# Performance work log

Hardware: AMD Instinct MI355X
Metric: run time of the kernel (lower is better)

## Reference

```python
import jax, jax.numpy as jnp
import numpy as np

NUM_NODES = 100000
NUM_EDGES = 1600000
NUM_GRAPHS = 128
D_IN, D_H1, D_H2, N_CLS = 128, 16, 128, 2


def gcn_conv(x, src, dst, W, b, num_nodes):
    # PyG GCNConv: linear transform, add self-loops, sym-normalized scatter-add
    h = x @ W  # [N, out]
    loop = jnp.arange(num_nodes, dtype=src.dtype)
    s = jnp.concatenate([src, loop])
    d = jnp.concatenate([dst, loop])
    deg = jax.ops.segment_sum(jnp.ones_like(d, dtype=h.dtype), d, num_segments=num_nodes)
    dinv = jax.lax.rsqrt(jnp.maximum(deg, 1.0))  # self-loops guarantee deg>=1
    norm = dinv[s] * dinv[d]  # [E+N]
    msg = h[s] * norm[:, None]  # gather + scale
    out = jax.ops.segment_sum(msg, d, num_segments=num_nodes)  # scatter-add
    return out + b


def setup_inputs() -> dict:
    key = jax.random.key(0)
    ks = jax.random.split(key, 12)
    x = jax.random.normal(ks[0], (NUM_NODES, D_IN), dtype=jnp.float32)
    edge_index = jax.random.randint(ks[1], (2, NUM_EDGES), 0, NUM_NODES, dtype=jnp.int64)
    batch = jax.random.randint(ks[2], (NUM_NODES,), 0, NUM_GRAPHS, dtype=jnp.int64)
    def glorot(k, shp):
        lim = np.sqrt(6.0 / (shp[0] + shp[1]))
        return jax.random.uniform(k, shp, dtype=jnp.float32, minval=-lim, maxval=lim)
    return {
        "x": x, "edge_index": edge_index, "batch": batch,
        "W1": glorot(ks[3], (D_IN, D_H1)), "b1": jnp.zeros((D_H1,), jnp.float32),
        "W2": glorot(ks[4], (D_H1, D_H2)), "b2": jnp.zeros((D_H2,), jnp.float32),
        "LW1": glorot(ks[5], (D_H2, D_H2)), "Lb1": jnp.zeros((D_H2,), jnp.float32),
        "LW2": glorot(ks[6], (D_H2, N_CLS)), "Lb2": jnp.zeros((N_CLS,), jnp.float32),
    }


def reference(x, edge_index, batch, W1, b1, W2, b2, LW1, Lb1, LW2, Lb2):
    src, dst = edge_index[0], edge_index[1]
    h = jax.nn.relu(gcn_conv(x, src, dst, W1, b1, NUM_NODES))
    h = jax.nn.relu(gcn_conv(h, src, dst, W2, b2, NUM_NODES))
    # global mean pool over graphs
    sums = jax.ops.segment_sum(h, batch, num_segments=NUM_GRAPHS)  # [G, D_H2]
    cnts = jax.ops.segment_sum(jnp.ones((h.shape[0],), h.dtype), batch, num_segments=NUM_GRAPHS)
    pooled = sums / jnp.maximum(cnts, 1.0)[:, None]
    z = jax.nn.relu(pooled @ LW1 + Lb1)
    z = z @ LW2 + Lb2
    return jax.nn.log_softmax(z, axis=-1)  # [G, num_classes]
```

## Files before the change

kernel.cpp:

```cpp
#include <hip/hip_runtime.h>

typedef unsigned int u32;

#define N_NODES  100000
#define N_EDGES  1600000
#define N_GRAPHS 128

#define NPB      200
#define NBUK     500
#define CHUNK    8192
#define NCHUNK   196
#define NHIST    (NBUK*NCHUNK)
#define NBLKA    383
#define CAP      6144

__global__ __launch_bounds__(512) void k_hist1(const int* __restrict__ dst, const int* __restrict__ batch,
                                               int* __restrict__ hist, int* __restrict__ bhist) {
    int t = threadIdx.x, b = blockIdx.x;
    if (b < NCHUNK) {
        __shared__ int lh[NBUK];
        for (int i = t; i < NBUK; i += 512) lh[i] = 0;
        __syncthreads();
        int base = b * CHUNK;
        #pragma unroll
        for (int it = 0; it < CHUNK / 512; ++it) {
            int e = base + it * 512 + t;
            if (e < N_EDGES) atomicAdd(&lh[dst[e] / NPB], 1);
        }
        __syncthreads();
        for (int i = t; i < NBUK; i += 512) hist[i * NCHUNK + b] = lh[i];
    } else {
        __shared__ int bh[N_GRAPHS];
        if (t < N_GRAPHS) bh[t] = 0;
        __syncthreads();
        int n = (b - NCHUNK) * 512 + t;
        if (n < N_NODES) atomicAdd(&bh[batch[n]], 1);
        __syncthreads();
        if (t < N_GRAPHS) atomicAdd(&bhist[t], bh[t]);
    }
}

__global__ __launch_bounds__(256) void k_scanA1(const int* __restrict__ hist, int* __restrict__ asum) {
    __shared__ int sh[256];
    int t = threadIdx.x, i = blockIdx.x * 256 + t;
    sh[t] = (i < NHIST) ? hist[i] : 0;
    __syncthreads();
    for (int off = 128; off > 0; off >>= 1) {
        if (t < off) sh[t] += sh[t + off];
        __syncthreads();
    }
    if (t == 0) asum[blockIdx.x] = sh[0];
}

__global__ __launch_bounds__(512) void k_scanA2(const int* __restrict__ asum, int* __restrict__ asumOff,
                                                const int* __restrict__ bhist, int* __restrict__ boff,
                                                int* __restrict__ bcur) {
    __shared__ int s1[512], s2[512];
    int t = threadIdx.x;
    int v = (t < NBLKA) ? asum[t] : 0;
    s1[t] = v; __syncthreads();
    int* pa = s1; int* pb = s2;
    for (int off = 1; off < 512; off <<= 1) {
        int x = pa[t];
        if (t >= off) x += pa[t - off];
        pb[t] = x; __syncthreads();
        int* tmp = pa; pa = pb; pb = tmp;
    }
    if (t < NBLKA) asumOff[t] = pa[t] - v;
    __syncthreads();
    int hv = (t < N_GRAPHS) ? bhist[t] : 0;
    pa[t] = hv; __syncthreads();
    int* qa = pa; int* qb = pb;
    for (int off = 1; off < 512; off <<= 1) {
        int x = qa[t];
        if (t >= off) x += qa[t - off];
        qb[t] = x; __syncthreads();
        int* tmp = qa; qa = qb; qb = tmp;
    }
    if (t < N_GRAPHS) { int e = qa[t] - hv; boff[t] = e; bcur[t] = e; }
    if (t == 0) boff[N_GRAPHS] = N_NODES;
}

__global__ __launch_bounds__(256) void k_scanA3(int* __restrict__ hist, const int* __restrict__ asumOff) {
    __shared__ int a1[256], a2[256];
    int t = threadIdx.x, i = blockIdx.x * 256 + t;
    int v = (i < NHIST) ? hist[i] : 0;
    a1[t] = v; __syncthreads();
    int* pa = a1; int* pb = a2;
    for (int off = 1; off < 256; off <<= 1) {
        int x = pa[t];
        if (t >= off) x += pa[t - off];
        pb[t] = x; __syncthreads();
        int* tmp = pa; pa = pb; pb = tmp;
    }
    if (i < NHIST) hist[i] = pa[t] - v + asumOff[blockIdx.x];
}

__global__ __launch_bounds__(512) void k_bin(const int* __restrict__ src, const int* __restrict__ dst,
                                             const int* __restrict__ hist, u32* __restrict__ packed,
                                             const int* __restrict__ batch, int* __restrict__ bcur,
                                             int* __restrict__ nodeS) {
    int t = threadIdx.x, b = blockIdx.x;
    if (b < NCHUNK) {
        __shared__ int cur5[NBUK];
        for (int i = t; i < NBUK; i += 512) cur5[i] = hist[i * NCHUNK + b];
        __syncthreads();
        int base = b * CHUNK;
        #pragma unroll
        for (int it = 0; it < CHUNK / 512; ++it) {
            int e = base + it * 512 + t;
            if (e < N_EDGES) {
                int d = dst[e], s = src[e];
                int bk = d / NPB;
                int pos = atomicAdd(&cur5[bk], 1);
                packed[pos] = ((u32)(d - bk * NPB) << 24) | (u32)s;
            }
        }
    } else {
        int n = (b - NCHUNK) * 512 + t;
        if (n < N_NODES) {
            int pos = atomicAdd(&bcur[batch[n]], 1);
            nodeS[pos] = n;
        }
    }
}

__global__ __launch_bounds__(256) void k_locCSR(const u32* __restrict__ packed, const int* __restrict__ hist,
                                                int* __restrict__ row, float* __restrict__ dinv,
                                                int* __restrict__ srcS) {
    __shared__ u32 lp[CAP];
    __shared__ int sbuf[CAP];
    __shared__ int cnt[NPB];
    __shared__ int s1[256], s2[256];
    int b = blockIdx.x, t = threadIdx.x;
    int start = hist[b * NCHUNK];
    int end   = (b == NBUK - 1) ? N_EDGES : hist[(b + 1) * NCHUNK];
    int len = end - start;
    for (int i = t; i < NPB; i += 256) cnt[i] = 0;
    __syncthreads();
    bool cached = (len <= CAP);
    if (cached) {
        for (int i = t; i < len; i += 256) {
            u32 p = packed[start + i];
            lp[i] = p;
            atomicAdd(&cnt[p >> 24], 1);
        }
    } else {
        for (int i = t; i < len; i += 256) {
            u32 p = packed[start + i];
            atomicAdd(&cnt[p >> 24], 1);
        }
    }
    __syncthreads();
    int v = (t < NPB) ? cnt[t] : 0;
    s1[t] = v; __syncthreads();
    int* pa = s1; int* pb = s2;
    for (int off = 1; off < 256; off <<= 1) {
        int x = pa[t];
        if (t >= off) x += pa[t - off];
        pb[t] = x; __syncthreads();
        int* tmp = pa; pa = pb; pb = tmp;
    }
    int excl = pa[t] - v;
    if (t < NPB) {
        row[b * NPB + t]  = start + excl;
        dinv[b * NPB + t] = rsqrtf((float)(v + 1));
    }
    if (b == NBUK - 1 && t == 0) row[N_NODES] = N_EDGES;
    __syncthreads();
    if (t < NPB) cnt[t] = excl;
    __syncthreads();
    if (cached) {
        for (int i = t; i < len; i += 256) {
            u32 p = lp[i];
            int lpos = atomicAdd(&cnt[p >> 24], 1);
            sbuf[lpos] = (int)(p & 0xFFFFFFu);
        }
        __syncthreads();
        for (int i = t; i < len; i += 256) srcS[start + i] = sbuf[i];
    } else {
        for (int i = t; i < len; i += 256) {
            u32 p = packed[start + i];
            int lpos = atomicAdd(&cnt[p >> 24], 1);
            srcS[start + lpos] = (int)(p & 0xFFFFFFu);
        }
    }
}

__global__ __launch_bounds__(256) void k_gemm1(const float* __restrict__ x, const float* __restrict__ W1,
                                               const float* __restrict__ dinv, float* __restrict__ t1s) {
    __shared__ float w[128 * 16];
    __shared__ float xs[16][132];
    int t = threadIdx.x;
    {
        const float4* wv = (const float4*)W1;
        ((float4*)w)[t * 2]     = wv[t * 2];
        ((float4*)w)[t * 2 + 1] = wv[t * 2 + 1];
    }
    int base = blockIdx.x * 16;
    {
        const float4* xv = (const float4*)(x + (size_t)base * 128);
        #pragma unroll
        for (int q = 0; q < 2; ++q) {
            int i4 = t * 2 + q;
            float4 v = xv[i4];
            int idx = i4 * 4;
            *((float4*)&xs[idx >> 7][idx & 127]) = v;
        }
    }
    __syncthreads();
    int nl = t >> 4, j = t & 15;
    int n = base + nl;
    const float4* xr = (const float4*)&xs[nl][0];
    float acc = 0.f;
    #pragma unroll
    for (int k4 = 0; k4 < 32; ++k4) {
        float4 v = xr[k4];
        acc += v.x * w[(k4 * 4 + 0) * 16 + j];
        acc += v.y * w[(k4 * 4 + 1) * 16 + j];
        acc += v.z * w[(k4 * 4 + 2) * 16 + j];
        acc += v.w * w[(k4 * 4 + 3) * 16 + j];
    }
    t1s[n * 16 + j] = dinv[n] * acc;
}

template <int LAYER>
__global__ __launch_bounds__(256) void k_gather(const int* __restrict__ row, const int* __restrict__ srcS,
                                                const float4* __restrict__ hs4, const float* __restrict__ dinv,
                                                const float* __restrict__ b1, float4* __restrict__ out4) {
    int t = threadIdx.x;
    int q = t & 3;
    int n = blockIdx.x * 64 + (t >> 2);
    if (n >= N_NODES) return;
    int r0 = row[n], r1 = row[n + 1];
    float4 a0 = hs4[(size_t)n * 4 + q];
    float4 a1 = {0.f, 0.f, 0.f, 0.f};
    float4 a2 = {0.f, 0.f, 0.f, 0.f};
    float4 a3 = {0.f, 0.f, 0.f, 0.f};
    int i = r0;
    for (; i + 4 <= r1; i += 4) {
        int s0 = srcS[i], s1 = srcS[i + 1], s2 = srcS[i + 2], s3 = srcS[i + 3];
        float4 v0 = hs4[(size_t)s0 * 4 + q];
        float4 v1 = hs4[(size_t)s1 * 4 + q];
        float4 v2 = hs4[(size_t)s2 * 4 + q];
        float4 v3 = hs4[(size_t)s3 * 4 + q];
        a0.x += v0.x; a0.y += v0.y; a0.z += v0.z; a0.w += v0.w;
        a1.x += v1.x; a1.y += v1.y; a1.z += v1.z; a1.w += v1.w;
        a2.x += v2.x; a2.y += v2.y; a2.z += v2.z; a2.w += v2.w;
        a3.x += v3.x; a3.y += v3.y; a3.z += v3.z; a3.w += v3.w;
    }
    for (; i < r1; ++i) {
        int s = srcS[i];
        float4 v = hs4[(size_t)s * 4 + q];
        a0.x += v.x; a0.y += v.y; a0.z += v.z; a0.w += v.w;
    }
    float sx = (a0.x + a1.x) + (a2.x + a3.x);
    float sy = (a0.y + a1.y) + (a2.y + a3.y);
    float sz = (a0.z + a1.z) + (a2.z + a3.z);
    float sw = (a0.w + a1.w) + (a2.w + a3.w);
    float dv = dinv[n];
    float4 r;
    if (LAYER == 1) {
        const float4 bb = ((const float4*)b1)[q];
        r.x = dv * fmaxf(dv * sx + bb.x, 0.f);
        r.y = dv * fmaxf(dv * sy + bb.y, 0.f);
        r.z = dv * fmaxf(dv * sz + bb.z, 0.f);
        r.w = dv * fmaxf(dv * sw + bb.w, 0.f);
    } else {
        r.x = dv * sx; r.y = dv * sy; r.z = dv * sz; r.w = dv * sw;
    }
    out4[(size_t)n * 4 + q] = r;
}

__global__ __launch_bounds__(256) void k_pool(const float* __restrict__ q2, const float* __restrict__ W2,
                                              const float* __restrict__ b2, const int* __restrict__ nodeS,
                                              const int* __restrict__ batch, float* __restrict__ sums) {
    __shared__ float w[16 * 128];
    __shared__ float bsh[128];
    __shared__ float rows[64][16];
    __shared__ int   gid[64];
    int t = threadIdx.x;
    {
        const float4* wv = (const float4*)W2;
        ((float4*)w)[t * 2]     = wv[t * 2];
        ((float4*)w)[t * 2 + 1] = wv[t * 2 + 1];
    }
    if (t < 128) bsh[t] = b2[t];
    int base = blockIdx.x * 64;
    {
        int which = t >> 2, qq = t & 3;
        int idx = base + which;
        if (idx < N_NODES) {
            int node = nodeS[idx];
            if (qq == 0) gid[which] = batch[node];
            float4 v = ((const float4*)q2)[(size_t)node * 4 + qq];
            *(float4*)&rows[which][qq * 4] = v;
        }
    }
    __syncthreads();
    int half = t >> 7, j = t & 127;
    float acc = 0.f;
    int curg = -1;
    for (int it = 0; it < 32; ++it) {
        int wh = half * 32 + it;
        int idx = base + wh;
        if (idx >= N_NODES) break;
        int g = gid[wh];
        if (g != curg) {
            if (curg >= 0) atomicAdd(&sums[curg * 128 + j], acc);
            curg = g; acc = 0.f;
        }
        float a = bsh[j];
        #pragma unroll
        for (int kk = 0; kk < 16; ++kk) a += rows[wh][kk] * w[kk * 128 + j];
        acc += fmaxf(a, 0.f);
    }
    if (curg >= 0) atomicAdd(&sums[curg * 128 + j], acc);
}

__global__ __launch_bounds__(128) void k_head(const float* __restrict__ sums, const int* __restrict__ boff,
                                              const float* __restrict__ LW1, const float* __restrict__ Lb1,
                                              const float* __restrict__ LW2, const float* __restrict__ Lb2,
                                              float* __restrict__ out) {
    __shared__ float srow[128];
    __shared__ float z1s[128];
    __shared__ float zz[2];
    int g = blockIdx.x, t = threadIdx.x;
    int cnt = boff[g + 1] - boff[g];
    float rc = 1.0f / fmaxf((float)cnt, 1.0f);
    srow[t] = sums[g * 128 + t] * rc;
    __syncthreads();
    float a = Lb1[t];
    for (int k = 0; k < 128; ++k) a += srow[k] * LW1[k * 128 + t];
    z1s[t] = fmaxf(a, 0.f);
    __syncthreads();
    if (t < 2) {
        float z = Lb2[t];
        for (int jj = 0; jj < 128; ++jj) z += z1s[jj] * LW2[jj * 2 + t];
        zz[t] = z;
    }
    __syncthreads();
    if (t < 2) {
        float m = fmaxf(zz[0], zz[1]);
        float lse = m + logf(expf(zz[0] - m) + expf(zz[1] - m));
        out[g * 2 + t] = zz[t] - lse;
    }
}

extern "C" void kernel_launch(void* const* d_in, const int* in_sizes, int n_in,
                              void* d_out, int out_size, void* d_ws, size_t ws_size,
                              hipStream_t stream) {
    const float* x   = (const float*)d_in[0];
    const int* ei    = (const int*)d_in[1];
    const int* batch = (const int*)d_in[2];
    const float* W1  = (const float*)d_in[3];
    const float* b1  = (const float*)d_in[4];
    const float* W2  = (const float*)d_in[5];
    const float* b2  = (const float*)d_in[6];
    const float* LW1 = (const float*)d_in[7];
    const float* Lb1 = (const float*)d_in[8];
    const float* LW2 = (const float*)d_in[9];
    const float* Lb2 = (const float*)d_in[10];
    const int* src = ei;
    const int* dst = ei + N_EDGES;

    char* ws = (char*)d_ws;
    int*   bhist   = (int*)(ws);
    float* sums    = (float*)(ws + 512);
    int*   bcur    = (int*)(ws + 66048);
    int*   boff    = (int*)(ws + 66560);
    int*   asum    = (int*)(ws + 67584);
    int*   asumOff = (int*)(ws + 69120);
    int*   hist    = (int*)(ws + 70656);
    int*   row     = (int*)(ws + 462656);
    float* dinv    = (float*)(ws + 862784);
    int*   nodeS   = (int*)(ws + 1262784);
    int*   srcS    = (int*)(ws + 1662784);
    u32*   packed  = (u32*)(ws + 8062784);
    float* A       = (float*)(ws + 8062784);
    float* B       = (float*)(ws + 14462784);
    float* out     = (float*)d_out;

    hipMemsetAsync(ws, 0, 66048, stream);

    k_hist1    <<<NCHUNK + 196, 512, 0, stream>>>(dst, batch, hist, bhist);
    k_scanA1   <<<NBLKA,        256, 0, stream>>>(hist, asum);
    k_scanA2   <<<1,            512, 0, stream>>>(asum, asumOff, bhist, boff, bcur);
    k_scanA3   <<<NBLKA,        256, 0, stream>>>(hist, asumOff);
    k_bin      <<<NCHUNK + 196, 512, 0, stream>>>(src, dst, hist, packed, batch, bcur, nodeS);
    k_locCSR   <<<NBUK,         256, 0, stream>>>(packed, hist, row, dinv, srcS);
    k_gemm1    <<<6250,         256, 0, stream>>>(x, W1, dinv, A);
    k_gather<1><<<1563,         256, 0, stream>>>(row, srcS, (const float4*)A, dinv, b1, (float4*)B);
    k_gather<2><<<1563,         256, 0, stream>>>(row, srcS, (const float4*)B, dinv, b1, (float4*)A);
    k_pool     <<<1563,         256, 0, stream>>>(A, W2, b2, nodeS, batch, sums);
    k_head     <<<128,          128, 0, stream>>>(sums, boff, LW1, Lb1, LW2, Lb2, out);
}
```

Measured before the change: 320.6 us.

## Replace per-node CSR gather with bucketed shared-memory scatter and fp16 features

Drops the local CSR build (row offsets, sorted srcS). Propagation now runs directly over the dst-bucketed packed edge list, accumulating into shared memory per 200-node bucket with LDS float atomics, then flushing to a global fp32 accumulator with global atomics. Node features are stored in fp16 to halve gather bandwidth, and a separate epilogue kernel applies the layer-1 bias/relu and rezeroes the accumulator. In exchange it adds global atomics, a large extra memset, fp16 rounding error, and a non-deterministic summation order.

```diff
diff --git a/kernel.cpp b/kernel.cpp
--- a/kernel.cpp
+++ b/kernel.cpp
@@ -1,6 +1,8 @@
 #include <hip/hip_runtime.h>
+#include <hip/hip_fp16.h>
 
 typedef unsigned int u32;
+typedef unsigned short u16;
 
 #define N_NODES  100000
 #define N_EDGES  1600000
@@ -12,7 +14,10 @@
 #define NCHUNK   196
 #define NHIST    (NBUK*NCHUNK)
 #define NBLKA    383
-#define CAP      6144
+#define NBN      196
+
+__device__ __forceinline__ float h2f(u16 h) { return __half2float(__ushort_as_half(h)); }
+__device__ __forceinline__ u16 f2h(float f) { return __half_as_ushort(__float2half_rn(f)); }
 
 __global__ __launch_bounds__(512) void k_hist1(const int* __restrict__ dst, const int* __restrict__ batch,
                                                int* __restrict__ hist, int* __restrict__ bhist) {
@@ -82,11 +87,11 @@
 }
 
 __global__ __launch_bounds__(256) void k_scanA3(int* __restrict__ hist, const int* __restrict__ asumOff) {
-    __shared__ int a1[256], a2[256];
+    __shared__ int s1[256], s2[256];
     int t = threadIdx.x, i = blockIdx.x * 256 + t;
     int v = (i < NHIST) ? hist[i] : 0;
-    a1[t] = v; __syncthreads();
-    int* pa = a1; int* pb = a2;
+    s1[t] = v; __syncthreads();
+    int* pa = s1; int* pb = s2;
     for (int off = 1; off < 256; off <<= 1) {
         int x = pa[t];
         if (t >= off) x += pa[t - off];
@@ -125,70 +130,21 @@
     }
 }
 
-__global__ __launch_bounds__(256) void k_locCSR(const u32* __restrict__ packed, const int* __restrict__ hist,
-                                                int* __restrict__ row, float* __restrict__ dinv,
-                                                int* __restrict__ srcS) {
-    __shared__ u32 lp[CAP];
-    __shared__ int sbuf[CAP];
+__global__ __launch_bounds__(256) void k_degdinv(const u32* __restrict__ packed, const int* __restrict__ hist,
+                                                 float* __restrict__ dinv) {
     __shared__ int cnt[NPB];
-    __shared__ int s1[256], s2[256];
     int b = blockIdx.x, t = threadIdx.x;
+    for (int i = t; i < NPB; i += 256) cnt[i] = 0;
+    __syncthreads();
     int start = hist[b * NCHUNK];
-    int end   = (b == NBUK - 1) ? N_EDGES : hist[(b + 1) * NCHUNK];
-    int len = end - start;
-    for (int i = t; i < NPB; i += 256) cnt[i] = 0;
-    __syncthreads();
-    bool cached = (len <= CAP);
-    if (cached) {
-        for (int i = t; i < len; i += 256) {
-            u32 p = packed[start + i];
-            lp[i] = p;
-            atomicAdd(&cnt[p >> 24], 1);
-        }
-    } else {
-        for (int i = t; i < len; i += 256) {
-            u32 p = packed[start + i];
-            atomicAdd(&cnt[p >> 24], 1);
-        }
-    }
-    __syncthreads();
-    int v = (t < NPB) ? cnt[t] : 0;
-    s1[t] = v; __syncthreads();
-    int* pa = s1; int* pb = s2;
-    for (int off = 1; off < 256; off <<= 1) {
-        int x = pa[t];
-        if (t >= off) x += pa[t - off];
-        pb[t] = x; __syncthreads();
-        int* tmp = pa; pa = pb; pb = tmp;
-    }
-    int excl = pa[t] - v;
-    if (t < NPB) {
-        row[b * NPB + t]  = start + excl;
-        dinv[b * NPB + t] = rsqrtf((float)(v + 1));
-    }
-    if (b == NBUK - 1 && t == 0) row[N_NODES] = N_EDGES;
-    __syncthreads();
-    if (t < NPB) cnt[t] = excl;
-    __syncthreads();
-    if (cached) {
-        for (int i = t; i < len; i += 256) {
-            u32 p = lp[i];
-            int lpos = atomicAdd(&cnt[p >> 24], 1);
-            sbuf[lpos] = (int)(p & 0xFFFFFFu);
-        }
-        __syncthreads();
-        for (int i = t; i < len; i += 256) srcS[start + i] = sbuf[i];
-    } else {
-        for (int i = t; i < len; i += 256) {
-            u32 p = packed[start + i];
-            int lpos = atomicAdd(&cnt[p >> 24], 1);
-            srcS[start + lpos] = (int)(p & 0xFFFFFFu);
-        }
-    }
+    int end = (b == NBUK - 1) ? N_EDGES : hist[(b + 1) * NCHUNK];
+    for (int i = start + t; i < end; i += 256) atomicAdd(&cnt[packed[i] >> 24], 1);
+    __syncthreads();
+    if (t < NPB) dinv[b * NPB + t] = rsqrtf((float)(cnt[t] + 1));
 }
 
 __global__ __launch_bounds__(256) void k_gemm1(const float* __restrict__ x, const float* __restrict__ W1,
-                                               const float* __restrict__ dinv, float* __restrict__ t1s) {
+                                               const float* __restrict__ dinv, u16* __restrict__ hs1) {
     __shared__ float w[128 * 16];
     __shared__ float xs[16][132];
     int t = threadIdx.x;
@@ -221,60 +177,69 @@
         acc += v.z * w[(k4 * 4 + 2) * 16 + j];
         acc += v.w * w[(k4 * 4 + 3) * 16 + j];
     }
-    t1s[n * 16 + j] = dinv[n] * acc;
-}
-
-template <int LAYER>
-__global__ __launch_bounds__(256) void k_gather(const int* __restrict__ row, const int* __restrict__ srcS,
-                                                const float4* __restrict__ hs4, const float* __restrict__ dinv,
-                                                const float* __restrict__ b1, float4* __restrict__ out4) {
+    hs1[n * 16 + j] = f2h(dinv[n] * acc);
+}
+
+__global__ __launch_bounds__(512) void k_prop(const u32* __restrict__ packed, const int* __restrict__ hist,
+                                              const u16* __restrict__ hs, float* __restrict__ pacc) {
+    __shared__ float acc[NPB][17];
     int t = threadIdx.x;
-    int q = t & 3;
-    int n = blockIdx.x * 64 + (t >> 2);
+    int b = blockIdx.x >> 1, half = blockIdx.x & 1;
+    for (int i = t; i < NPB * 17; i += 512) (&acc[0][0])[i] = 0.f;
+    __syncthreads();
+    int start = hist[b * NCHUNK];
+    int end = (b == NBUK - 1) ? N_EDGES : hist[(b + 1) * NCHUNK];
+    int mid = start + ((end - start) >> 1);
+    int r0 = half ? mid : start;
+    int r1 = half ? end : mid;
+    int g = t >> 2, q = t & 3;
+    for (int i = r0 + g; i < r1; i += 128) {
+        u32 p = packed[i];
+        int dloc = (int)(p >> 24);
+        int s = (int)(p & 0xFFFFFFu);
+        ushort4 v = ((const ushort4*)hs)[s * 4 + q];
+        int c = q * 4;
+        atomicAdd(&acc[dloc][c + 0], h2f(v.x));
+        atomicAdd(&acc[dloc][c + 1], h2f(v.y));
+        atomicAdd(&acc[dloc][c + 2], h2f(v.z));
+        atomicAdd(&acc[dloc][c + 3], h2f(v.w));
+    }
+    __syncthreads();
+    int nb = b * NPB;
+    for (int i = t; i < NPB * 16; i += 512) {
+        int r = i >> 4, c = i & 15;
+        float v = acc[r][c];
+        if (v != 0.f) atomicAdd(&pacc[(nb + r) * 16 + c], v);
+    }
+}
+
+__global__ __launch_bounds__(256) void k_epi1(float* __restrict__ pacc, const u16* __restrict__ hs1,
+                                              const float* __restrict__ dinv, const float* __restrict__ b1,
+                                              u16* __restrict__ hs2) {
+    int gid = blockIdx.x * 256 + threadIdx.x;
+    int n = gid >> 2, q = gid & 3;
     if (n >= N_NODES) return;
-    int r0 = row[n], r1 = row[n + 1];
-    float4 a0 = hs4[(size_t)n * 4 + q];
-    float4 a1 = {0.f, 0.f, 0.f, 0.f};
-    float4 a2 = {0.f, 0.f, 0.f, 0.f};
-    float4 a3 = {0.f, 0.f, 0.f, 0.f};
-    int i = r0;
-    for (; i + 4 <= r1; i += 4) {
-        int s0 = srcS[i], s1 = srcS[i + 1], s2 = srcS[i + 2], s3 = srcS[i + 3];
-        float4 v0 = hs4[(size_t)s0 * 4 + q];
-        float4 v1 = hs4[(size_t)s1 * 4 + q];
-        float4 v2 = hs4[(size_t)s2 * 4 + q];
-        float4 v3 = hs4[(size_t)s3 * 4 + q];
-        a0.x += v0.x; a0.y += v0.y; a0.z += v0.z; a0.w += v0.w;
-        a1.x += v1.x; a1.y += v1.y; a1.z += v1.z; a1.w += v1.w;
-        a2.x += v2.x; a2.y += v2.y; a2.z += v2.z; a2.w += v2.w;
-        a3.x += v3.x; a3.y += v3.y; a3.z += v3.z; a3.w += v3.w;
-    }
-    for (; i < r1; ++i) {
-        int s = srcS[i];
-        float4 v = hs4[(size_t)s * 4 + q];
-        a0.x += v.x; a0.y += v.y; a0.z += v.z; a0.w += v.w;
-    }
-    float sx = (a0.x + a1.x) + (a2.x + a3.x);
-    float sy = (a0.y + a1.y) + (a2.y + a3.y);
-    float sz = (a0.z + a1.z) + (a2.z + a3.z);
-    float sw = (a0.w + a1.w) + (a2.w + a3.w);
+    int base = n * 4 + q;
+    float4 pv = ((float4*)pacc)[base];
+    ushort4 hv = ((const ushort4*)hs1)[base];
+    float4 bb = ((const float4*)b1)[q];
     float dv = dinv[n];
-    float4 r;
-    if (LAYER == 1) {
-        const float4 bb = ((const float4*)b1)[q];
-        r.x = dv * fmaxf(dv * sx + bb.x, 0.f);
-        r.y = dv * fmaxf(dv * sy + bb.y, 0.f);
-        r.z = dv * fmaxf(dv * sz + bb.z, 0.f);
-        r.w = dv * fmaxf(dv * sw + bb.w, 0.f);
-    } else {
-        r.x = dv * sx; r.y = dv * sy; r.z = dv * sz; r.w = dv * sw;
-    }
-    out4[(size_t)n * 4 + q] = r;
-}
-
-__global__ __launch_bounds__(256) void k_pool(const float* __restrict__ q2, const float* __restrict__ W2,
-                                              const float* __restrict__ b2, const int* __restrict__ nodeS,
-                                              const int* __restrict__ batch, float* __restrict__ sums) {
+    float h0 = fmaxf(dv * (pv.x + h2f(hv.x)) + bb.x, 0.f);
+    float h1 = fmaxf(dv * (pv.y + h2f(hv.y)) + bb.y, 0.f);
+    float h2 = fmaxf(dv * (pv.z + h2f(hv.z)) + bb.z, 0.f);
+    float h3 = fmaxf(dv * (pv.w + h2f(hv.w)) + bb.w, 0.f);
+    ushort4 o;
+    o.x = f2h(dv * h0); o.y = f2h(dv * h1); o.z = f2h(dv * h2); o.w = f2h(dv * h3);
+    ((ushort4*)hs2)[base] = o;
+    float4 z = {0.f, 0.f, 0.f, 0.f};
+    ((float4*)pacc)[base] = z;
+}
+
+__global__ __launch_bounds__(256) void k_pool(const float* __restrict__ pacc, const u16* __restrict__ hs2,
+                                              const float* __restrict__ dinv,
+                                              const float* __restrict__ W2, const float* __restrict__ b2,
+                                              const int* __restrict__ nodeS, const int* __restrict__ batch,
+                                              float* __restrict__ sums) {
     __shared__ float w[16 * 128];
     __shared__ float bsh[128];
     __shared__ float rows[64][16];
@@ -293,8 +258,13 @@
         if (idx < N_NODES) {
             int node = nodeS[idx];
             if (qq == 0) gid[which] = batch[node];
-            float4 v = ((const float4*)q2)[(size_t)node * 4 + qq];
-            *(float4*)&rows[which][qq * 4] = v;
+            float dv = dinv[node];
+            float4 pv = ((const float4*)pacc)[node * 4 + qq];
+            ushort4 hv = ((const ushort4*)hs2)[node * 4 + qq];
+            rows[which][qq * 4 + 0] = dv * (pv.x + h2f(hv.x));
+            rows[which][qq * 4 + 1] = dv * (pv.y + h2f(hv.y));
+            rows[which][qq * 4 + 2] = dv * (pv.z + h2f(hv.z));
+            rows[which][qq * 4 + 3] = dv * (pv.w + h2f(hv.w));
         }
     }
     __syncthreads();
@@ -367,31 +337,31 @@
     char* ws = (char*)d_ws;
     int*   bhist   = (int*)(ws);
     float* sums    = (float*)(ws + 512);
-    int*   bcur    = (int*)(ws + 66048);
-    int*   boff    = (int*)(ws + 66560);
-    int*   asum    = (int*)(ws + 67584);
-    int*   asumOff = (int*)(ws + 69120);
-    int*   hist    = (int*)(ws + 70656);
-    int*   row     = (int*)(ws + 462656);
-    float* dinv    = (float*)(ws + 862784);
-    int*   nodeS   = (int*)(ws + 1262784);
-    int*   srcS    = (int*)(ws + 1662784);
-    u32*   packed  = (u32*)(ws + 8062784);
-    float* A       = (float*)(ws + 8062784);
-    float* B       = (float*)(ws + 14462784);
+    float* pacc    = (float*)(ws + 66048);
+    int*   bcur    = (int*)(ws + 6466048);
+    int*   boff    = (int*)(ws + 6466560);
+    int*   asum    = (int*)(ws + 6467584);
+    int*   asumOff = (int*)(ws + 6469120);
+    int*   hist    = (int*)(ws + 6470656);
+    float* dinv    = (float*)(ws + 6862656);
+    int*   nodeS   = (int*)(ws + 7262656);
+    u32*   packed  = (u32*)(ws + 7662656);
+    u16*   hs1     = (u16*)(ws + 14062656);
+    u16*   hs2     = (u16*)(ws + 17262656);
     float* out     = (float*)d_out;
 
-    hipMemsetAsync(ws, 0, 66048, stream);
-
-    k_hist1    <<<NCHUNK + 196, 512, 0, stream>>>(dst, batch, hist, bhist);
-    k_scanA1   <<<NBLKA,        256, 0, stream>>>(hist, asum);
-    k_scanA2   <<<1,            512, 0, stream>>>(asum, asumOff, bhist, boff, bcur);
-    k_scanA3   <<<NBLKA,        256, 0, stream>>>(hist, asumOff);
-    k_bin      <<<NCHUNK + 196, 512, 0, stream>>>(src, dst, hist, packed, batch, bcur, nodeS);
-    k_locCSR   <<<NBUK,         256, 0, stream>>>(packed, hist, row, dinv, srcS);
-    k_gemm1    <<<6250,         256, 0, stream>>>(x, W1, dinv, A);
-    k_gather<1><<<1563,         256, 0, stream>>>(row, srcS, (const float4*)A, dinv, b1, (float4*)B);
-    k_gather<2><<<1563,         256, 0, stream>>>(row, srcS, (const float4*)B, dinv, b1, (float4*)A);
-    k_pool     <<<1563,         256, 0, stream>>>(A, W2, b2, nodeS, batch, sums);
-    k_head     <<<128,          128, 0, stream>>>(sums, boff, LW1, Lb1, LW2, Lb2, out);
-}
+    hipMemsetAsync(ws, 0, 6466048, stream);
+
+    k_hist1  <<<NCHUNK + NBN, 512, 0, stream>>>(dst, batch, hist, bhist);
+    k_scanA1 <<<NBLKA,        256, 0, stream>>>(hist, asum);
+    k_scanA2 <<<1,            512, 0, stream>>>(asum, asumOff, bhist, boff, bcur);
+    k_scanA3 <<<NBLKA,        256, 0, stream>>>(hist, asumOff);
+    k_bin    <<<NCHUNK + NBN, 512, 0, stream>>>(src, dst, hist, packed, batch, bcur, nodeS);
+    k_degdinv<<<NBUK,         256, 0, stream>>>(packed, hist, dinv);
+    k_gemm1  <<<6250,         256, 0, stream>>>(x, W1, dinv, hs1);
+    k_prop   <<<2 * NBUK,     512, 0, stream>>>(packed, hist, hs1, pacc);
+    k_epi1   <<<1563,         256, 0, stream>>>(pacc, hs1, dinv, b1, hs2);
+    k_prop   <<<2 * NBUK,     512, 0, stream>>>(packed, hist, hs2, pacc);
+    k_pool   <<<1563,         256, 0, stream>>>(pacc, hs2, dinv, W2, b2, nodeS, batch, sums);
+    k_head   <<<128,          128, 0, stream>>>(sums, boff, LW1, Lb1, LW2, Lb2, out);
+}
```

Result: slower. 545.6 us (+70.2%).
